# Optimization experiments

Hardware: AMD Instinct MI355X
Metric: run time of the kernel (lower is better)

The kernel has to match this reference:

```python
import jax, jax.numpy as jnp
import numpy as np

B, S, HID, NH = 2, 2048, 1024, 16
HD = HID // NH
SCALE = HD ** -0.5


def elu_plus_one(x):
    return jax.nn.elu(x) + 1.0


def setup_inputs() -> dict:
    key = jax.random.key(0)
    ks = jax.random.split(key, 8)
    w_scale = 0.02  # keep logits in a sane range
    return {
        "hidden_states": jax.random.normal(ks[0], (B, S, HID), jnp.float32),
        "wq": jax.random.normal(ks[1], (HID, HID), jnp.float32) * w_scale,
        "wk": jax.random.normal(ks[2], (HID, HID), jnp.float32) * w_scale,
        "wv": jax.random.normal(ks[3], (HID, HID), jnp.float32) * w_scale,
        "wo": jax.random.normal(ks[4], (HID, HID), jnp.float32) * w_scale,
        "beta": jax.random.normal(ks[5], (NH,), jnp.float32),
        "memory": jax.random.normal(ks[6], (NH, HD, HD), jnp.float32),
        "memory_norm": jax.random.uniform(ks[7], (NH, HD), jnp.float32),
    }


def reference(hidden_states, wq, wk, wv, wo, beta, memory, memory_norm):
    b, s, _ = hidden_states.shape
    # nn.Linear(bias=False): x @ W^T; weights stored [out, in]
    def proj(x, w):
        return jnp.einsum("bsh,oh->bso", x, w).reshape(b, s, NH, HD).transpose(0, 2, 1, 3)

    q = proj(hidden_states, wq)  # [B,H,S,D]
    k = proj(hidden_states, wk)
    v = proj(hidden_states, wv)

    # local causal softmax attention (materializes [B,H,S,S] as the original does)
    scores = jnp.einsum("bhsd,bhtd->bhst", q, k) * SCALE
    causal_mask = jnp.triu(jnp.full((s, s), -jnp.inf, dtype=scores.dtype), k=1)
    attn = jax.nn.softmax(scores + causal_mask, axis=-1)
    a_local = jnp.einsum("bhst,bhtd->bhsd", attn, v)

    # compressive memory retrieval: sigma(Q) @ M / (sigma(Q) @ z)
    sigma_q = elu_plus_one(q)
    a_mem_unnorm = jnp.einsum("bhsd,hde->bhse", sigma_q, memory)
    norm = jnp.clip(jnp.einsum("bhsd,hd->bhs", sigma_q, memory_norm), 1e-6, None)
    a_mem = a_mem_unnorm / norm[..., None]

    gate = jax.nn.sigmoid(beta).reshape(1, NH, 1, 1)
    combined = gate * a_mem + (1.0 - gate) * a_local  # [B,H,S,D]
    combined = combined.transpose(0, 2, 1, 3).reshape(b, s, HID)
    return jnp.einsum("bsh,oh->bso", combined, wo)
```

## Files before the change

kernel.cpp:

```cpp
#include <hip/hip_runtime.h>
#include <stdint.h>

#define LOG2E 1.4426950408889634f

typedef __attribute__((ext_vector_type(8))) __bf16 bf16x8;
typedef __attribute__((ext_vector_type(4))) __bf16 bf16x4;
typedef __attribute__((ext_vector_type(4))) float f32x4;

__device__ inline void gll16(const void* g, void* l) {
  __builtin_amdgcn_global_load_lds(
      (const __attribute__((address_space(1))) void*)g,
      (__attribute__((address_space(3))) void*)l, 16, 0, 0);
}

__global__ __launch_bounds__(256) void cvt_all(
    const float* __restrict__ hs, const float* __restrict__ wq,
    const float* __restrict__ wk, const float* __restrict__ wv,
    const float* __restrict__ wo,
    __bf16* __restrict__ hsb, __bf16* __restrict__ wqb, __bf16* __restrict__ wkb,
    __bf16* __restrict__ wvb, __bf16* __restrict__ wob) {
  int bid = blockIdx.x;
  const float* s; __bf16* d; int i;
  if (bid < 4096) { s = hs; d = hsb; i = bid * 256 + threadIdx.x; }
  else {
    int seg = (bid - 4096) >> 10;
    i = ((bid - 4096) & 1023) * 256 + threadIdx.x;
    s = seg == 0 ? wq : seg == 1 ? wk : seg == 2 ? wv : wo;
    d = seg == 0 ? wqb : seg == 1 ? wkb : seg == 2 ? wvb : wob;
  }
  float4 v = ((const float4*)s)[i];
  bf16x4 o;
  o[0] = (__bf16)v.x; o[1] = (__bf16)v.y; o[2] = (__bf16)v.z; o[3] = (__bf16)v.w;
  *(bf16x4*)&d[(size_t)i * 4] = o;
}

#define KSCALE 0.18033688011112042f
__global__ __launch_bounds__(256, 3) void qkv_gemm(
    const __bf16* __restrict__ hsb, const __bf16* __restrict__ wqb,
    const __bf16* __restrict__ wkb, const __bf16* __restrict__ wvb,
    __bf16* __restrict__ qbuf, __bf16* __restrict__ kbuf,
    __bf16* __restrict__ vtb) {
  constexpr int K = 1024;
  __shared__ __align__(16) __bf16 lta[128 * 32];
  __shared__ __align__(16) __bf16 ltb[128 * 32];
  const int bid = blockIdx.x;
  const int z = bid >> 8, r = bid & 255;
  const __bf16 *A, *Bt;
  int m0, n0;
  if (z < 2) {
    A = hsb; Bt = z ? wkb : wqb;
    m0 = (r & 31) * 128; n0 = (r >> 5) * 128;
  } else {
    A = wvb; Bt = hsb;
    m0 = (r & 7) * 128; n0 = (r >> 3) * 128;
  }
  const int tid = threadIdx.x;
  const int w = tid >> 6, l = tid & 63;
  const int lg = l >> 4, lr = l & 15;
  const int wm = (w >> 1) * 64, wn = (w & 1) * 64;
  f32x4 acc[4][4] = {};
  const int srow = w * 16 + (l >> 2);
  const int scol = (l & 3) * 8;
  const __bf16* ga = A + (size_t)(m0 + srow) * K + scol;
  const __bf16* gb = Bt + (size_t)(n0 + srow) * K + scol;
  __bf16* la = &lta[(size_t)w * 16 * 32];
  __bf16* lb = &ltb[(size_t)w * 16 * 32];
  for (int k0 = 0; k0 < K; k0 += 32) {
    __syncthreads();
    gll16(ga + k0, la);
    gll16(ga + 64 * K + k0, la + 64 * 32);
    gll16(gb + k0, lb);
    gll16(gb + 64 * K + k0, lb + 64 * 32);
    __syncthreads();
    bf16x8 af[4], bfr[4];
#pragma unroll
    for (int i = 0; i < 4; ++i) {
      af[i]  = *(const bf16x8*)&lta[(wm + i * 16 + lr) * 32 + lg * 8];
      bfr[i] = *(const bf16x8*)&ltb[(wn + i * 16 + lr) * 32 + lg * 8];
    }
#pragma unroll
    for (int i = 0; i < 4; ++i)
#pragma unroll
      for (int j = 0; j < 4; ++j)
        acc[i][j] = __builtin_amdgcn_mfma_f32_16x16x32_bf16(af[i], bfr[j], acc[i][j], 0, 0, 0);
  }
#pragma unroll
  for (int i = 0; i < 4; ++i)
#pragma unroll
    for (int j = 0; j < 4; ++j)
#pragma unroll
      for (int rr = 0; rr < 4; ++rr) {
        int gm = m0 + wm + i * 16 + lg * 4 + rr;
        int gn = n0 + wn + j * 16 + lr;
        float v = acc[i][j][rr];
        if (z < 2) {
          int bb = gm >> 11, s = gm & 2047, hh = gn >> 6, d = gn & 63;
          __bf16* dst = z ? kbuf : qbuf;
          if (z) v *= KSCALE;
          dst[(((size_t)bb * 16 + hh) * 2048 + s) * 64 + d] = (__bf16)v;
        } else {
          int bb = gn >> 11, s = gn & 2047, hh = gm >> 6, d = gm & 63;
          vtb[(((size_t)bb * 16 + hh) * 64 + d) * 2048 + s] = (__bf16)v;
        }
      }
}

__global__ __launch_bounds__(256, 2) void gemm_out(const __bf16* __restrict__ A,
                                                   const __bf16* __restrict__ Bt,
                                                   float* __restrict__ C,
                                                   int M, int N) {
  constexpr int K = 1024;
  __shared__ __align__(16) __bf16 lta[128 * 32];
  __shared__ __align__(16) __bf16 ltb[128 * 32];
  const int tid = threadIdx.x;
  const int w = tid >> 6, l = tid & 63;
  const int lg = l >> 4, lr = l & 15;
  const int m0 = blockIdx.x * 128, n0 = blockIdx.y * 128;
  const int wm = (w >> 1) * 64, wn = (w & 1) * 64;
  f32x4 acc[4][4] = {};
  const int srow = w * 16 + (l >> 2);
  const int scol = (l & 3) * 8;
  const __bf16* ga = A + (size_t)(m0 + srow) * K + scol;
  const __bf16* gb = Bt + (size_t)(n0 + srow) * K + scol;
  __bf16* la = &lta[(size_t)w * 16 * 32];
  __bf16* lb = &ltb[(size_t)w * 16 * 32];
  for (int k0 = 0; k0 < K; k0 += 32) {
    __syncthreads();
    gll16(ga + k0, la);
    gll16(ga + 64 * K + k0, la + 64 * 32);
    gll16(gb + k0, lb);
    gll16(gb + 64 * K + k0, lb + 64 * 32);
    __syncthreads();
    bf16x8 af[4], bfr[4];
#pragma unroll
    for (int i = 0; i < 4; ++i) {
      af[i]  = *(const bf16x8*)&lta[(wm + i * 16 + lr) * 32 + lg * 8];
      bfr[i] = *(const bf16x8*)&ltb[(wn + i * 16 + lr) * 32 + lg * 8];
    }
#pragma unroll
    for (int i = 0; i < 4; ++i)
#pragma unroll
      for (int j = 0; j < 4; ++j)
        acc[i][j] = __builtin_amdgcn_mfma_f32_16x16x32_bf16(af[i], bfr[j], acc[i][j], 0, 0, 0);
  }
#pragma unroll
  for (int i = 0; i < 4; ++i)
#pragma unroll
    for (int j = 0; j < 4; ++j)
#pragma unroll
      for (int rr = 0; rr < 4; ++rr) {
        int gm = m0 + wm + i * 16 + lg * 4 + rr;
        int gn = n0 + wn + j * 16 + lr;
        C[(size_t)gm * N + gn] = acc[i][j][rr];
      }
}

#define MTP 72
#define DEFER_THR 11.5f
#define SWZ(row, col) (((row) << 7) + ((col) ^ (((row) & 7) << 3)))
#define SWZK(row, col) (((row) << 6) + ((col) ^ (((row) & 7) << 3)))

__global__ __launch_bounds__(256, 3) void attn_kernel(
    const __bf16* __restrict__ qb,
    const __bf16* __restrict__ kb,
    const __bf16* __restrict__ vtb,
    const float* __restrict__ memory,
    const float* __restrict__ memnorm,
    const float* __restrict__ beta,
    __bf16* __restrict__ comb)
{
  __shared__ __align__(16) __bf16 kt[128 * 64];
  __shared__ __align__(16) __bf16 vt[64 * 128];
  __shared__ __align__(16) __bf16 pt[64 * 128];

  const int tid = threadIdx.x;
  const int w = tid >> 6, l = tid & 63;
  const int lg = l >> 4, lr = l & 15;
  const int bx = blockIdx.x;
  const int t = 31 - (bx >> 5);
  const int bh = bx & 31;
  const int hh = bh & 15, b = bh >> 4;
  const int wq0 = t * 64 + w * 16;
  const int ntiles = (t >> 1) + 1;

  const int s_sk = tid >> 3, s_d8 = (tid & 7) * 8;
  const int s_d = tid >> 4, s_sk8 = (tid & 15) * 8;
  const __bf16* kbase = kb + ((size_t)bh * 2048 + s_sk) * 64 + s_d8;
  const __bf16* vbase = vtb + ((size_t)bh * 64 + s_d) * 2048 + s_sk8;

  bf16x8 qf[2];
#pragma unroll
  for (int kk = 0; kk < 2; ++kk)
    qf[kk] = *(const bf16x8*)(qb + ((size_t)bh * 2048 + wq0 + lr) * 64 + kk * 32 + lg * 8);

  bf16x8 kst[4], vst[4];
#pragma unroll
  for (int is = 0; is < 4; ++is) {
    kst[is] = *(const bf16x8*)(kbase + (size_t)is * 32 * 64);
    vst[is] = *(const bf16x8*)(vbase + is * 16 * 2048);
  }

  float mrun = -1e30f, lsum = 0.f;
  f32x4 apv[4] = {};

  for (int kv = 0; kv < ntiles; ++kv) {
    const int kv0 = kv * 128;
    __syncthreads();
#pragma unroll
    for (int is = 0; is < 4; ++is) {
      *(bf16x8*)&kt[SWZK(s_sk + is * 32, s_d8)] = kst[is];
      *(bf16x8*)&vt[SWZ(s_d + is * 16, s_sk8)] = vst[is];
    }
    __syncthreads();
    if (kv + 1 < ntiles) {
      const size_t off = (size_t)(kv + 1) * 128;
#pragma unroll
      for (int is = 0; is < 4; ++is) {
        kst[is] = *(const bf16x8*)(kbase + ((size_t)is * 32) * 64 + off * 64);
        vst[is] = *(const bf16x8*)(vbase + is * 16 * 2048 + off);
      }
    }

    f32x4 sc[8] = {};
#pragma unroll
    for (int kk = 0; kk < 2; ++kk)
#pragma unroll
      for (int nf = 0; nf < 8; ++nf) {
        bf16x8 kf = *(const bf16x8*)&kt[SWZK(nf * 16 + lr, kk * 32 + lg * 8)];
        sc[nf] = __builtin_amdgcn_mfma_f32_16x16x32_bf16(kf, qf[kk], sc[nf], 0, 0, 0);
      }

    const int qrow = wq0 + lr;
    if (kv0 + 127 > wq0) {
#pragma unroll
      for (int nf = 0; nf < 8; ++nf)
#pragma unroll
        for (int r = 0; r < 4; ++r)
          if (kv0 + nf * 16 + lg * 4 + r > qrow) sc[nf][r] = -1e30f;
    }
    f32x4 m4 = sc[0];
#pragma unroll
    for (int nf = 1; nf < 8; ++nf)
#pragma unroll
      for (int r = 0; r < 4; ++r) m4[r] = fmaxf(m4[r], sc[nf][r]);
    float mx = fmaxf(fmaxf(m4[0], m4[1]), fmaxf(m4[2], m4[3]));
    mx = fmaxf(mx, __shfl_xor(mx, 16, 64));
    mx = fmaxf(mx, __shfl_xor(mx, 32, 64));

    if (!__all(mx - mrun <= DEFER_THR)) {
      float mold = mrun;
      float mn = fmaxf(mold, mx);
      mrun = mn;
      float scl = __builtin_amdgcn_exp2f(mold - mn);
      lsum *= scl;
      float sclq[4];
#pragma unroll
      for (int r = 0; r < 4; ++r) sclq[r] = __shfl(scl, (lg << 2) | r, 16);
#pragma unroll
      for (int nf = 0; nf < 4; ++nf)
#pragma unroll
        for (int r = 0; r < 4; ++r) apv[nf][r] *= sclq[r];
    }

    float rs = 0.f;
#pragma unroll
    for (int nf = 0; nf < 8; ++nf) {
      bf16x4 pk;
#pragma unroll
      for (int r = 0; r < 4; ++r) {
        float pv = __builtin_amdgcn_exp2f(sc[nf][r] - mrun);
        rs += pv;
        pk[r] = (__bf16)pv;
      }
      *(bf16x4*)&pt[SWZ(w * 16 + lr, nf * 16 + lg * 4)] = pk;
    }
    rs += __shfl_xor(rs, 16, 64);
    rs += __shfl_xor(rs, 32, 64);
    lsum += rs;

#pragma unroll
    for (int kk = 0; kk < 4; ++kk) {
      bf16x8 pa = *(const bf16x8*)&pt[SWZ(w * 16 + lr, kk * 32 + lg * 8)];
#pragma unroll
      for (int nf = 0; nf < 4; ++nf) {
        bf16x8 vf = *(const bf16x8*)&vt[SWZ(nf * 16 + lr, kk * 32 + lg * 8)];
        apv[nf] = __builtin_amdgcn_mfma_f32_16x16x32_bf16(pa, vf, apv[nf], 0, 0, 0);
      }
    }
  }

  __syncthreads();
  __bf16* mt = kt;
  for (int i = tid; i < 64 * 64; i += 256) {
    int d = i >> 6, e = i & 63;
    mt[e * MTP + d] = (__bf16)memory[((size_t)hh * 64 + d) * 64 + e];
  }
  for (int i = tid; i < 16 * 64; i += 256) {
    int e = 64 + (i >> 6), d = i & 63;
    mt[e * MTP + d] = (__bf16)memnorm[hh * 64 + d];
  }
  __syncthreads();

  bf16x8 sf[2];
#pragma unroll
  for (int kk = 0; kk < 2; ++kk) {
    bf16x8 q = qf[kk], s;
#pragma unroll
    for (int j = 0; j < 8; ++j) {
      float x = (float)q[j];
      float sg = x > 0.f ? x + 1.f : __builtin_amdgcn_exp2f(x * LOG2E);
      s[j] = (__bf16)sg;
    }
    sf[kk] = s;
  }

  f32x4 am[5] = {};
#pragma unroll
  for (int kk = 0; kk < 2; ++kk)
#pragma unroll
    for (int nf = 0; nf < 5; ++nf) {
      bf16x8 bb = *(const bf16x8*)&mt[(nf * 16 + lr) * MTP + kk * 32 + lg * 8];
      am[nf] = __builtin_amdgcn_mfma_f32_16x16x32_bf16(sf[kk], bb, am[nf], 0, 0, 0);
    }

  const float gate = 1.f / (1.f + __builtin_amdgcn_exp2f(-beta[hh] * LOG2E));
  const float og = 1.f - gate;
  float lsq[4];
#pragma unroll
  for (int r = 0; r < 4; ++r) lsq[r] = __shfl(lsum, (lg << 2) | r, 16);
#pragma unroll
  for (int r = 0; r < 4; ++r) {
    int row = wq0 + lg * 4 + r;
    float linv = __builtin_amdgcn_rcpf(lsq[r]);
    float nrm = fmaxf(am[4][r], 1e-6f);
    float ninv = __builtin_amdgcn_rcpf(nrm);
    size_t base = ((size_t)b * 2048 + row) * 1024 + hh * 64;
#pragma unroll
    for (int nf = 0; nf < 4; ++nf) {
      float al = apv[nf][r] * linv;
      float amv = am[nf][r] * ninv;
      comb[base + nf * 16 + lr] = (__bf16)(gate * amv + og * al);
    }
  }
}

extern "C" void kernel_launch(void* const* d_in, const int* in_sizes, int n_in,
                              void* d_out, int out_size, void* d_ws, size_t ws_size,
                              hipStream_t stream) {
  const float* hs      = (const float*)d_in[0];
  const float* wq      = (const float*)d_in[1];
  const float* wk      = (const float*)d_in[2];
  const float* wv      = (const float*)d_in[3];
  const float* wo      = (const float*)d_in[4];
  const float* beta    = (const float*)d_in[5];
  const float* memory  = (const float*)d_in[6];
  const float* memnorm = (const float*)d_in[7];
  float* out = (float*)d_out;

  char* ws = (char*)d_ws;
  __bf16* hsb  = (__bf16*)(ws);
  __bf16* wqb  = (__bf16*)(ws + ((size_t)8  << 20));
  __bf16* wkb  = (__bf16*)(ws + ((size_t)10 << 20));
  __bf16* wvb  = (__bf16*)(ws + ((size_t)12 << 20));
  __bf16* wob  = (__bf16*)(ws + ((size_t)14 << 20));
  __bf16* qbuf = (__bf16*)(ws + ((size_t)16 << 20));
  __bf16* kbuf = (__bf16*)(ws + ((size_t)24 << 20));
  __bf16* vtb  = (__bf16*)(ws + ((size_t)32 << 20));
  __bf16* comb = (__bf16*)(ws + ((size_t)40 << 20));

  cvt_all<<<8192, 256, 0, stream>>>(hs, wq, wk, wv, wo, hsb, wqb, wkb, wvb, wob);

  qkv_gemm<<<768, 256, 0, stream>>>(hsb, wqb, wkb, wvb, qbuf, kbuf, vtb);

  attn_kernel<<<1024, 256, 0, stream>>>(qbuf, kbuf, vtb, memory, memnorm, beta, comb);

  gemm_out<<<dim3(32, 8), 256, 0, stream>>>(comb, wob, out, 4096, 1024);
}
```

Before: 110.3 us.

## Load attention K/V tiles via global_load_lds and keep P in registers

In the attention kernel, the register-staged K/V prefetch is replaced with direct global-to-LDS loads, using source-side XOR swizzling so the tiles land in the existing swizzled layout. The probability tile no longer goes through shared memory: it is packed to bf16 with v_cvt_pk and redistributed across lanes with permlane32 swaps and shuffles. Dropping the P buffer and the staging registers lets occupancy rise to 5 blocks, and causal masking now applies only to the last tile. Separately, the output GEMM uses 128x64 tiles to launch twice as many blocks. The trade-offs are the loss of the register prefetch overlap for K/V and extra lane-shuffle instructions per tile.

New measurement: 110.2 us. No clear change (-0.1%).

```diff
diff --git a/kernel.cpp b/kernel.cpp
--- a/kernel.cpp
+++ b/kernel.cpp
@@ -111,42 +111,42 @@
                                                    int M, int N) {
   constexpr int K = 1024;
   __shared__ __align__(16) __bf16 lta[128 * 32];
-  __shared__ __align__(16) __bf16 ltb[128 * 32];
+  __shared__ __align__(16) __bf16 ltb[64 * 32];
   const int tid = threadIdx.x;
   const int w = tid >> 6, l = tid & 63;
   const int lg = l >> 4, lr = l & 15;
-  const int m0 = blockIdx.x * 128, n0 = blockIdx.y * 128;
-  const int wm = (w >> 1) * 64, wn = (w & 1) * 64;
-  f32x4 acc[4][4] = {};
-  const int srow = w * 16 + (l >> 2);
-  const int scol = (l & 3) * 8;
+  const int m0 = blockIdx.x * 128, n0 = blockIdx.y * 64;
+  const int wm = (w >> 1) * 64, wn = (w & 1) * 32;
+  f32x4 acc[4][2] = {};
+  const int srow = tid >> 2;
+  const int scol = (tid & 3) * 8;
   const __bf16* ga = A + (size_t)(m0 + srow) * K + scol;
   const __bf16* gb = Bt + (size_t)(n0 + srow) * K + scol;
-  __bf16* la = &lta[(size_t)w * 16 * 32];
-  __bf16* lb = &ltb[(size_t)w * 16 * 32];
+  __bf16* la = &lta[(size_t)w * 512];
+  __bf16* lb = &ltb[(size_t)w * 512];
   for (int k0 = 0; k0 < K; k0 += 32) {
     __syncthreads();
     gll16(ga + k0, la);
-    gll16(ga + 64 * K + k0, la + 64 * 32);
+    gll16(ga + (size_t)64 * K + k0, la + 64 * 32);
     gll16(gb + k0, lb);
-    gll16(gb + 64 * K + k0, lb + 64 * 32);
-    __syncthreads();
-    bf16x8 af[4], bfr[4];
-#pragma unroll
-    for (int i = 0; i < 4; ++i) {
+    __syncthreads();
+    bf16x8 af[4], bfr[2];
+#pragma unroll
+    for (int i = 0; i < 4; ++i)
       af[i]  = *(const bf16x8*)&lta[(wm + i * 16 + lr) * 32 + lg * 8];
-      bfr[i] = *(const bf16x8*)&ltb[(wn + i * 16 + lr) * 32 + lg * 8];
-    }
+#pragma unroll
+    for (int j = 0; j < 2; ++j)
+      bfr[j] = *(const bf16x8*)&ltb[(wn + j * 16 + lr) * 32 + lg * 8];
 #pragma unroll
     for (int i = 0; i < 4; ++i)
 #pragma unroll
-      for (int j = 0; j < 4; ++j)
+      for (int j = 0; j < 2; ++j)
         acc[i][j] = __builtin_amdgcn_mfma_f32_16x16x32_bf16(af[i], bfr[j], acc[i][j], 0, 0, 0);
   }
 #pragma unroll
   for (int i = 0; i < 4; ++i)
 #pragma unroll
-    for (int j = 0; j < 4; ++j)
+    for (int j = 0; j < 2; ++j)
 #pragma unroll
       for (int rr = 0; rr < 4; ++rr) {
         int gm = m0 + wm + i * 16 + lg * 4 + rr;
@@ -155,12 +155,11 @@
       }
 }
 
-#define MTP 72
 #define DEFER_THR 11.5f
 #define SWZ(row, col) (((row) << 7) + ((col) ^ (((row) & 7) << 3)))
 #define SWZK(row, col) (((row) << 6) + ((col) ^ (((row) & 7) << 3)))
 
-__global__ __launch_bounds__(256, 3) void attn_kernel(
+__global__ __launch_bounds__(256, 5) void attn_kernel(
     const __bf16* __restrict__ qb,
     const __bf16* __restrict__ kb,
     const __bf16* __restrict__ vtb,
@@ -171,35 +170,30 @@
 {
   __shared__ __align__(16) __bf16 kt[128 * 64];
   __shared__ __align__(16) __bf16 vt[64 * 128];
-  __shared__ __align__(16) __bf16 pt[64 * 128];
 
   const int tid = threadIdx.x;
   const int w = tid >> 6, l = tid & 63;
   const int lg = l >> 4, lr = l & 15;
-  const int bx = blockIdx.x;
-  const int t = 31 - (bx >> 5);
-  const int bh = bx & 31;
+  const int t = 31 - (blockIdx.x >> 5);
+  const int bh = blockIdx.x & 31;
   const int hh = bh & 15, b = bh >> 4;
   const int wq0 = t * 64 + w * 16;
   const int ntiles = (t >> 1) + 1;
 
-  const int s_sk = tid >> 3, s_d8 = (tid & 7) * 8;
-  const int s_d = tid >> 4, s_sk8 = (tid & 15) * 8;
-  const __bf16* kbase = kb + ((size_t)bh * 2048 + s_sk) * 64 + s_d8;
-  const __bf16* vbase = vtb + ((size_t)bh * 64 + s_d) * 2048 + s_sk8;
+  const int k_row = tid >> 3;
+  const int k_col = ((tid & 7) ^ (k_row & 7)) * 8;
+  const __bf16* ksrc = kb + ((size_t)bh * 2048 + k_row) * 64 + k_col;
+  const int v_d = tid >> 4;
+  const int v_col = ((tid & 15) ^ (v_d & 7)) * 8;
+  const __bf16* vsrc = vtb + ((size_t)bh * 64 + v_d) * 2048 + v_col;
+  __bf16* kdst = &kt[w * 512];
+  __bf16* vdst = &vt[w * 512];
 
   bf16x8 qf[2];
 #pragma unroll
   for (int kk = 0; kk < 2; ++kk)
     qf[kk] = *(const bf16x8*)(qb + ((size_t)bh * 2048 + wq0 + lr) * 64 + kk * 32 + lg * 8);
 
-  bf16x8 kst[4], vst[4];
-#pragma unroll
-  for (int is = 0; is < 4; ++is) {
-    kst[is] = *(const bf16x8*)(kbase + (size_t)is * 32 * 64);
-    vst[is] = *(const bf16x8*)(vbase + is * 16 * 2048);
-  }
-
   float mrun = -1e30f, lsum = 0.f;
   f32x4 apv[4] = {};
 
@@ -207,19 +201,11 @@
     const int kv0 = kv * 128;
     __syncthreads();
 #pragma unroll
-    for (int is = 0; is < 4; ++is) {
-      *(bf16x8*)&kt[SWZK(s_sk + is * 32, s_d8)] = kst[is];
-      *(bf16x8*)&vt[SWZ(s_d + is * 16, s_sk8)] = vst[is];
-    }
-    __syncthreads();
-    if (kv + 1 < ntiles) {
-      const size_t off = (size_t)(kv + 1) * 128;
-#pragma unroll
-      for (int is = 0; is < 4; ++is) {
-        kst[is] = *(const bf16x8*)(kbase + ((size_t)is * 32) * 64 + off * 64);
-        vst[is] = *(const bf16x8*)(vbase + is * 16 * 2048 + off);
-      }
-    }
+    for (int i = 0; i < 4; ++i) {
+      gll16(ksrc + (size_t)(kv0 + i * 32) * 64, kdst + i * 2048);
+      gll16(vsrc + (size_t)i * 16 * 2048 + kv0, vdst + i * 2048);
+    }
+    __syncthreads();
 
     f32x4 sc[8] = {};
 #pragma unroll
@@ -231,13 +217,14 @@
       }
 
     const int qrow = wq0 + lr;
-    if (kv0 + 127 > wq0) {
+    if (kv == ntiles - 1) {
 #pragma unroll
       for (int nf = 0; nf < 8; ++nf)
 #pragma unroll
         for (int r = 0; r < 4; ++r)
           if (kv0 + nf * 16 + lg * 4 + r > qrow) sc[nf][r] = -1e30f;
     }
+
     f32x4 m4 = sc[0];
 #pragma unroll
     for (int nf = 1; nf < 8; ++nf)
@@ -262,29 +249,43 @@
         for (int r = 0; r < 4; ++r) apv[nf][r] *= sclq[r];
     }
 
-    float rs = 0.f;
-#pragma unroll
-    for (int nf = 0; nf < 8; ++nf) {
-      bf16x4 pk;
+    f32x4 rs4 = {0.f, 0.f, 0.f, 0.f};
+#pragma unroll
+    for (int nf = 0; nf < 8; ++nf)
 #pragma unroll
       for (int r = 0; r < 4; ++r) {
         float pv = __builtin_amdgcn_exp2f(sc[nf][r] - mrun);
-        rs += pv;
-        pk[r] = (__bf16)pv;
-      }
-      *(bf16x4*)&pt[SWZ(w * 16 + lr, nf * 16 + lg * 4)] = pk;
-    }
+        sc[nf][r] = pv;
+        rs4[r] += pv;
+      }
+    float rs = (rs4[0] + rs4[1]) + (rs4[2] + rs4[3]);
     rs += __shfl_xor(rs, 16, 64);
     rs += __shfl_xor(rs, 32, 64);
     lsum += rs;
 
 #pragma unroll
     for (int kk = 0; kk < 4; ++kk) {
-      bf16x8 pa = *(const bf16x8*)&pt[SWZ(w * 16 + lr, kk * 32 + lg * 8)];
+      uint32_t a0, a1, b0, b1;
+      asm("v_cvt_pk_bf16_f32 %0, %1, %2" : "=v"(a0) : "v"(sc[2 * kk][0]), "v"(sc[2 * kk][1]));
+      asm("v_cvt_pk_bf16_f32 %0, %1, %2" : "=v"(a1) : "v"(sc[2 * kk][2]), "v"(sc[2 * kk][3]));
+      asm("v_cvt_pk_bf16_f32 %0, %1, %2" : "=v"(b0) : "v"(sc[2 * kk + 1][0]), "v"(sc[2 * kk + 1][1]));
+      asm("v_cvt_pk_bf16_f32 %0, %1, %2" : "=v"(b1) : "v"(sc[2 * kk + 1][2]), "v"(sc[2 * kk + 1][3]));
+      asm("v_permlane32_swap_b32 %0, %1" : "+v"(a0), "+v"(b0));
+      asm("v_permlane32_swap_b32 %0, %1" : "+v"(a1), "+v"(b1));
+      uint32_t sx0 = (uint32_t)__shfl_xor((int)a0, 16, 64);
+      uint32_t sy0 = (uint32_t)__shfl_xor((int)b0, 16, 64);
+      uint32_t sx1 = (uint32_t)__shfl_xor((int)a1, 16, 64);
+      uint32_t sy1 = (uint32_t)__shfl_xor((int)b1, 16, 64);
+      const bool odd = (lg & 1);
+      union { uint32_t u[4]; bf16x8 v; } pa;
+      pa.u[0] = odd ? sy0 : a0;
+      pa.u[1] = odd ? sy1 : a1;
+      pa.u[2] = odd ? b0 : sx0;
+      pa.u[3] = odd ? b1 : sx1;
 #pragma unroll
       for (int nf = 0; nf < 4; ++nf) {
         bf16x8 vf = *(const bf16x8*)&vt[SWZ(nf * 16 + lr, kk * 32 + lg * 8)];
-        apv[nf] = __builtin_amdgcn_mfma_f32_16x16x32_bf16(pa, vf, apv[nf], 0, 0, 0);
+        apv[nf] = __builtin_amdgcn_mfma_f32_16x16x32_bf16(pa.v, vf, apv[nf], 0, 0, 0);
       }
     }
   }
@@ -293,11 +294,11 @@
   __bf16* mt = kt;
   for (int i = tid; i < 64 * 64; i += 256) {
     int d = i >> 6, e = i & 63;
-    mt[e * MTP + d] = (__bf16)memory[((size_t)hh * 64 + d) * 64 + e];
+    mt[e * 72 + d] = (__bf16)memory[((size_t)hh * 64 + d) * 64 + e];
   }
   for (int i = tid; i < 16 * 64; i += 256) {
     int e = 64 + (i >> 6), d = i & 63;
-    mt[e * MTP + d] = (__bf16)memnorm[hh * 64 + d];
+    mt[e * 72 + d] = (__bf16)memnorm[hh * 64 + d];
   }
   __syncthreads();
 
@@ -319,7 +320,7 @@
   for (int kk = 0; kk < 2; ++kk)
 #pragma unroll
     for (int nf = 0; nf < 5; ++nf) {
-      bf16x8 bb = *(const bf16x8*)&mt[(nf * 16 + lr) * MTP + kk * 32 + lg * 8];
+      bf16x8 bb = *(const bf16x8*)&mt[(nf * 16 + lr) * 72 + kk * 32 + lg * 8];
       am[nf] = __builtin_amdgcn_mfma_f32_16x16x32_bf16(sf[kk], bb, am[nf], 0, 0, 0);
     }
 
@@ -374,5 +375,5 @@
 
   attn_kernel<<<1024, 256, 0, stream>>>(qbuf, kbuf, vtb, memory, memnorm, beta, comb);
 
-  gemm_out<<<dim3(32, 8), 256, 0, stream>>>(comb, wob, out, 4096, 1024);
-}
+  gemm_out<<<dim3(32, 16), 256, 0, stream>>>(comb, wob, out, 4096, 1024);
+}
```
